# Optimization experiments

Measured on AMD Instinct MI355X. Metric: run time of the kernel, lower is better.

Reference implementation:

```python
import jax, jax.numpy as jnp
import numpy as np

HEADS = 8
TQ, QH, QW = 4, 16, 16
TK, KH, KW = 4, 16, 16
DIM = 64


def setup_inputs() -> dict:
    key = jax.random.key(0)
    k1, k2, k3, k4, k5 = jax.random.split(key, 5)
    return {
        "query": jax.random.normal(k1, (4, HEADS, TQ * QH * QW, DIM), dtype=jnp.float32),
        "scores": jax.random.normal(k2, (4, HEADS, TQ * QH * QW, TK * KH * KW), dtype=jnp.float32),
        "height_embeddings": jax.random.normal(k3, (2 * (max(QH, KH) - 1) + 1, DIM), dtype=jnp.float32),
        "width_embeddings": jax.random.normal(k4, (2 * (max(QW, KW) - 1) + 1, DIM), dtype=jnp.float32),
        "time_embeddings": jax.random.normal(k5, (2 * (max(TQ, TK) - 1) + 1, DIM), dtype=jnp.float32),
    }


def _rel_dist(q_n, k_n):
    # matches torch: ratios are both 1 when q_n == k_n
    q_ratio = round(max(k_n / q_n, 1.0))
    k_ratio = round(max(q_n / k_n, 1.0))
    d = jnp.arange(q_n)[:, None] * q_ratio - jnp.arange(k_n)[None, :] * k_ratio
    return d + (k_n - 1) * k_ratio  # [q_n, k_n] int indices


def reference(query, scores, height_embeddings, width_embeddings, time_embeddings):
    Rh = height_embeddings[_rel_dist(QH, KH)]  # [QH, KH, DIM]
    Rw = width_embeddings[_rel_dist(QW, KW)]   # [QW, KW, DIM]
    Rt = time_embeddings[_rel_dist(TQ, TK)]    # [TQ, TK, DIM]

    q = query.reshape(-1, HEADS, TQ, QH, QW, DIM)
    rel_h = jnp.einsum('bNthwc,hkc->bNthwk', q, Rh)  # [B,N,T,H,W,KH]
    rel_w = jnp.einsum('bNthwc,wkc->bNthwk', q, Rw)  # [B,N,T,H,W,KW]
    rel_t = jnp.einsum('bNthwc,tkc->bNthwk', q, Rt)  # [B,N,T,H,W,TK]

    s = scores.reshape(-1, HEADS, TQ, QH, QW, TK, KH, KW)
    s = (s
         + rel_h[:, :, :, :, :, None, :, None]
         + rel_w[:, :, :, :, :, None, None, :]
         + rel_t[:, :, :, :, :, :, None, None])
    return s.reshape(-1, HEADS, TQ * QH * QW, TK * KH * KW)
```

## Files before the change

### kernel.cpp

```cpp
#include <hip/hip_runtime.h>

#define NHEADS 8
#define TQ 4
#define QH 16
#define QW 16
#define TK 4
#define KH 16
#define KW 16
#define DIM 64
#define BATCH 4

#define ROWS (BATCH * NHEADS * TQ * QH * QW)
#define RPB 16
#define EST 68

typedef float f4 __attribute__((ext_vector_type(4)));

__global__ __launch_bounds__(256) void relpos_stage_kernel(
    const float* __restrict__ query,
    const float* __restrict__ scores,
    const float* __restrict__ hemb,
    const float* __restrict__ wemb,
    const float* __restrict__ temb,
    float* __restrict__ out)
{
    const int tid  = threadIdx.x;
    const int lane = tid & 63;
    const int wv   = tid >> 6;
    const int row0 = blockIdx.x * RPB;
    const int pos  = row0 & 1023;
    const int t = pos >> 8;
    const int h = (pos >> 4) & 15;

    __shared__ float lds_q[RPB][EST];
    __shared__ float lds_h[16][EST];
    __shared__ float lds_w[31][EST];
    __shared__ float lds_t[4][EST];
    __shared__ float rel[RPB][40];

    {
        const f4* sq = (const f4*)(query + (size_t)row0 * DIM);
        const f4* sh = (const f4*)(hemb + (size_t)h * DIM);
        const f4* sw = (const f4*)wemb;
        const f4* st = (const f4*)(temb + (size_t)t * DIM);
        {
            const int r = tid >> 4, c = tid & 15;
            *(f4*)&lds_q[r][4 * c] = sq[tid];
            *(f4*)&lds_h[r][4 * c] = sh[tid];
            *(f4*)&lds_w[r][4 * c] = sw[tid];
        }
        if (tid < 240) {
            const int k = 256 + tid;
            *(f4*)&lds_w[k >> 4][4 * (k & 15)] = sw[k];
        }
        if (tid < 64)
            *(f4*)&lds_t[tid >> 4][4 * (tid & 15)] = st[tid];
    }
    __syncthreads();

    const size_t rbase = (size_t)(row0 + wv * 4) * 1024;
    f4 s[4][4];
#pragma unroll
    for (int r = 0; r < 4; ++r) {
        const f4* sp = (const f4*)(scores + rbase + (size_t)r * 1024);
#pragma unroll
        for (int i = 0; i < 4; ++i)
            s[r][i] = sp[lane + 64 * i];
    }

#pragma unroll
    for (int d0 = 0; d0 < 144; d0 += 64) {
        const int d = d0 + lane;
        if (d < 144) {
            const int rl  = d / 36;
            const int j   = d - rl * 36;
            const int row = wv * 4 + rl;
            const float* ep;
            if (j < 16)      ep = &lds_h[15 - j][0];
            else if (j < 32) ep = &lds_w[row - (j - 16) + 15][0];
            else             ep = &lds_t[3 - (j - 32)][0];
            const float* qp = &lds_q[row][0];
            float acc = 0.f;
#pragma unroll
            for (int c = 0; c < 16; ++c) {
                f4 qv = *(const f4*)(qp + 4 * c);
                f4 ev = *(const f4*)(ep + 4 * c);
                acc += qv.x * ev.x + qv.y * ev.y + qv.z * ev.z + qv.w * ev.w;
            }
            rel[row][j] = acc;
        }
    }

    const int kh  = lane >> 2;
    const int kw0 = (lane << 2) & 15;
#pragma unroll
    for (int r = 0; r < 4; ++r) {
        const int row = wv * 4 + r;
        const float hv = rel[row][kh];
        const f4 tv  = *(const f4*)&rel[row][32];
        const f4 wv4 = *(const f4*)&rel[row][16 + kw0];
        f4* op = (f4*)(out + rbase + (size_t)r * 1024);
#pragma unroll
        for (int i = 0; i < 4; ++i) {
            f4 o = s[r][i] + (hv + tv[i]) + wv4;
            __builtin_nontemporal_store(o, op + lane + 64 * i);
        }
    }
}

extern "C" void kernel_launch(void* const* d_in, const int* in_sizes, int n_in,
                              void* d_out, int out_size, void* d_ws, size_t ws_size,
                              hipStream_t stream) {
    const float* query  = (const float*)d_in[0];
    const float* scores = (const float*)d_in[1];
    const float* hemb   = (const float*)d_in[2];
    const float* wemb   = (const float*)d_in[3];
    const float* temb   = (const float*)d_in[4];
    float* out = (float*)d_out;

    relpos_stage_kernel<<<dim3(ROWS / RPB), dim3(256), 0, stream>>>(
        query, scores, hemb, wemb, temb, out);
}
```

Baseline: 247.2 us.

## Process 64 rows per block with double-buffered score loads overlapping compute

Each block now covers four times as many rows, and each wave streams its 16 rows in four epochs through two register buffers. Score loads for the first two epochs are issued before the shared-memory staging and the dot-product stage, and later epochs are loaded while earlier ones are stored. The aim is to hide global memory latency and amortise embedding staging across more rows. The cost is higher register pressure, fewer blocks, and larger shared memory use, which may lower occupancy.

```diff
diff --git a/kernel.cpp b/kernel.cpp
--- a/kernel.cpp
+++ b/kernel.cpp
@@ -11,12 +11,12 @@
 #define BATCH 4
 
 #define ROWS (BATCH * NHEADS * TQ * QH * QW)
-#define RPB 16
+#define RPB 64
 #define EST 68
 
 typedef float f4 __attribute__((ext_vector_type(4)));
 
-__global__ __launch_bounds__(256) void relpos_stage_kernel(
+__global__ __launch_bounds__(256) void relpos_pipe_kernel(
     const float* __restrict__ query,
     const float* __restrict__ scores,
     const float* __restrict__ hemb,
@@ -29,83 +29,98 @@
     const int wv   = tid >> 6;
     const int row0 = blockIdx.x * RPB;
     const int pos  = row0 & 1023;
-    const int t = pos >> 8;
-    const int h = (pos >> 4) & 15;
+    const int t  = pos >> 8;
+    const int h0 = (pos >> 4) & 15;
 
     __shared__ float lds_q[RPB][EST];
-    __shared__ float lds_h[16][EST];
+    __shared__ float lds_h[19][EST];
     __shared__ float lds_w[31][EST];
     __shared__ float lds_t[4][EST];
     __shared__ float rel[RPB][40];
 
+    const int kh  = lane >> 2;
+    const int kw0 = (lane & 3) << 2;
+
+    const f4* sp = (const f4*)scores + (size_t)(row0 + wv * 16) * 256;
+    f4*       op = (f4*)out          + (size_t)(row0 + wv * 16) * 256;
+
+    f4 A[4][4], B[4][4];
+
+    auto epoch_load = [&](f4 buf[4][4], int e) {
+#pragma unroll
+        for (int r = 0; r < 4; ++r)
+#pragma unroll
+            for (int i = 0; i < 4; ++i)
+                buf[r][i] = __builtin_nontemporal_load(sp + (e * 4 + r) * 256 + lane + 64 * i);
+    };
+    auto epoch_store = [&](f4 buf[4][4], int e) {
+#pragma unroll
+        for (int r = 0; r < 4; ++r) {
+            const int lr = wv * 16 + e * 4 + r;
+            const float hv = rel[lr][kh];
+            const f4 tv = *(const f4*)&rel[lr][32];
+            const f4 w4 = *(const f4*)&rel[lr][16 + kw0];
+#pragma unroll
+            for (int i = 0; i < 4; ++i) {
+                f4 o = buf[r][i] + (hv + tv[i]) + w4;
+                __builtin_nontemporal_store(o, op + (e * 4 + r) * 256 + lane + 64 * i);
+            }
+        }
+    };
+
+    epoch_load(A, 0);
+    epoch_load(B, 1);
+
     {
         const f4* sq = (const f4*)(query + (size_t)row0 * DIM);
-        const f4* sh = (const f4*)(hemb + (size_t)h * DIM);
+        const f4* sh = (const f4*)(hemb + (size_t)h0 * DIM);
         const f4* sw = (const f4*)wemb;
         const f4* st = (const f4*)(temb + (size_t)t * DIM);
+#pragma unroll
+        for (int k0 = 0; k0 < 1024; k0 += 256) {
+            const int k = k0 + tid;
+            *(f4*)&lds_q[k >> 4][4 * (k & 15)] = sq[k];
+        }
+        if (tid < 304 - 256) { const int k = 256 + tid; *(f4*)&lds_h[k >> 4][4 * (k & 15)] = sh[k]; }
+        { const int k = tid; if (k < 304) {} }
         {
-            const int r = tid >> 4, c = tid & 15;
-            *(f4*)&lds_q[r][4 * c] = sq[tid];
-            *(f4*)&lds_h[r][4 * c] = sh[tid];
-            *(f4*)&lds_w[r][4 * c] = sw[tid];
+            const int k = tid;
+            if (k < 256) *(f4*)&lds_h[k >> 4][4 * (k & 15)] = sh[k];
         }
-        if (tid < 240) {
-            const int k = 256 + tid;
+        {
+            const int k = tid;
             *(f4*)&lds_w[k >> 4][4 * (k & 15)] = sw[k];
+            if (k < 496 - 256) { const int k2 = 256 + k; *(f4*)&lds_w[k2 >> 4][4 * (k2 & 15)] = sw[k2]; }
         }
-        if (tid < 64)
-            *(f4*)&lds_t[tid >> 4][4 * (tid & 15)] = st[tid];
+        if (tid < 64) *(f4*)&lds_t[tid >> 4][4 * (tid & 15)] = st[tid];
     }
     __syncthreads();
 
-    const size_t rbase = (size_t)(row0 + wv * 4) * 1024;
-    f4 s[4][4];
+    for (int d = lane; d < 576; d += 64) {
+        const int rr = d / 36;
+        const int j  = d - rr * 36;
+        const int lr = wv * 16 + rr;
+        const float* ep;
+        if (j < 16)      ep = &lds_h[wv + 15 - j][0];
+        else if (j < 32) ep = &lds_w[rr - (j - 16) + 15][0];
+        else             ep = &lds_t[3 - (j - 32)][0];
+        const float* qp = &lds_q[lr][0];
+        float acc = 0.f;
 #pragma unroll
-    for (int r = 0; r < 4; ++r) {
-        const f4* sp = (const f4*)(scores + rbase + (size_t)r * 1024);
-#pragma unroll
-        for (int i = 0; i < 4; ++i)
-            s[r][i] = sp[lane + 64 * i];
+        for (int c = 0; c < 16; ++c) {
+            f4 qv = *(const f4*)(qp + 4 * c);
+            f4 ev = *(const f4*)(ep + 4 * c);
+            acc += qv.x * ev.x + qv.y * ev.y + qv.z * ev.z + qv.w * ev.w;
+        }
+        rel[lr][j] = acc;
     }
 
-#pragma unroll
-    for (int d0 = 0; d0 < 144; d0 += 64) {
-        const int d = d0 + lane;
-        if (d < 144) {
-            const int rl  = d / 36;
-            const int j   = d - rl * 36;
-            const int row = wv * 4 + rl;
-            const float* ep;
-            if (j < 16)      ep = &lds_h[15 - j][0];
-            else if (j < 32) ep = &lds_w[row - (j - 16) + 15][0];
-            else             ep = &lds_t[3 - (j - 32)][0];
-            const float* qp = &lds_q[row][0];
-            float acc = 0.f;
-#pragma unroll
-            for (int c = 0; c < 16; ++c) {
-                f4 qv = *(const f4*)(qp + 4 * c);
-                f4 ev = *(const f4*)(ep + 4 * c);
-                acc += qv.x * ev.x + qv.y * ev.y + qv.z * ev.z + qv.w * ev.w;
-            }
-            rel[row][j] = acc;
-        }
-    }
-
-    const int kh  = lane >> 2;
-    const int kw0 = (lane << 2) & 15;
-#pragma unroll
-    for (int r = 0; r < 4; ++r) {
-        const int row = wv * 4 + r;
-        const float hv = rel[row][kh];
-        const f4 tv  = *(const f4*)&rel[row][32];
-        const f4 wv4 = *(const f4*)&rel[row][16 + kw0];
-        f4* op = (f4*)(out + rbase + (size_t)r * 1024);
-#pragma unroll
-        for (int i = 0; i < 4; ++i) {
-            f4 o = s[r][i] + (hv + tv[i]) + wv4;
-            __builtin_nontemporal_store(o, op + lane + 64 * i);
-        }
-    }
+    epoch_store(A, 0);
+    epoch_load (A, 2);
+    epoch_store(B, 1);
+    epoch_load (B, 3);
+    epoch_store(A, 2);
+    epoch_store(B, 3);
 }
 
 extern "C" void kernel_launch(void* const* d_in, const int* in_sizes, int n_in,
@@ -118,6 +133,6 @@
     const float* temb   = (const float*)d_in[4];
     float* out = (float*)d_out;
 
-    relpos_stage_kernel<<<dim3(ROWS / RPB), dim3(256), 0, stream>>>(
+    relpos_pipe_kernel<<<dim3(ROWS / RPB), dim3(256), 0, stream>>>(
         query, scores, hemb, wemb, temb, out);
 }
```

Result: no change. 245.3 us (-0.8%).
